# Performance work log

Hardware: AMD Instinct MI355X
Metric: run time of the kernel (lower is better)

The kernel has to match this reference:

```python
import jax, jax.numpy as jnp
import numpy as np
import math

DIM = 1024
P0 = 512          # num_stored_patterns
H = 16            # num_heads
HD = DIM // H     # head_dim = 64
STEPS = 3
B, S = 2, 1024
NEG = -1e9


def sparsemax(z):
    # sort descending along last axis
    z_sorted = -jnp.sort(-z, axis=-1)
    z_cumsum = jnp.cumsum(z_sorted, axis=-1)
    k = jnp.arange(1, z.shape[-1] + 1, dtype=z.dtype)
    support = (1 + k * z_sorted > z_cumsum).astype(z.dtype)
    k_max = support.sum(axis=-1, keepdims=True)
    idx = jnp.clip(k_max - 1, 0, None).astype(jnp.int32)
    tau = (jnp.take_along_axis(z_cumsum, idx, axis=-1) - 1.0) / jnp.maximum(k_max, 1.0)
    return jnp.clip(z - tau, 0.0, None)


def setup_inputs() -> dict:
    key = jax.random.key(0)
    ks = jax.random.split(key, 12)
    z_real = jax.random.normal(ks[0], (B, S, DIM), dtype=jnp.float32)
    z_imag = jax.random.normal(ks[1], (B, S, DIM), dtype=jnp.float32)
    # causal additive mask over dynamic (sequence) patterns
    mask = jnp.where(jnp.tril(jnp.ones((S, S), dtype=bool)), 0.0, NEG).astype(jnp.float32)
    sc = 1.0 / math.sqrt(DIM)
    stored_patterns = jax.random.normal(ks[2], (P0, DIM), dtype=jnp.float32) * 0.02
    Wq = jax.random.normal(ks[3], (DIM, DIM), dtype=jnp.float32) * sc
    Wk = jax.random.normal(ks[4], (DIM, DIM), dtype=jnp.float32) * sc
    Wv = jax.random.normal(ks[5], (DIM, DIM), dtype=jnp.float32) * sc
    Wo = jax.random.normal(ks[6], (2 * DIM, DIM), dtype=jnp.float32) * sc
    bo = jnp.zeros((2 * DIM,), dtype=jnp.float32)
    log_temp = jax.random.normal(ks[7], (H,), dtype=jnp.float32) * 0.1  # temperature=1 -> log 0
    gamma = jnp.ones((2 * DIM,), dtype=jnp.float32)
    beta = jnp.zeros((2 * DIM,), dtype=jnp.float32)
    return {"z_real": z_real, "z_imag": z_imag, "mask": mask,
            "stored_patterns": stored_patterns, "Wq": Wq, "Wk": Wk, "Wv": Wv,
            "Wo": Wo, "bo": bo, "log_temp": log_temp, "gamma": gamma, "beta": beta}


def reference(z_real, z_imag, mask, stored_patterns, Wq, Wk, Wv, Wo, bo, log_temp, gamma, beta):
    Bz, Sz, D = z_real.shape
    mag = jnp.sqrt(z_real * z_real + z_imag * z_imag)           # |z| -> dynamic patterns
    learned = jnp.broadcast_to(stored_patterns[None], (Bz, P0, D))
    patterns = jnp.concatenate([learned, mag], axis=1)          # (B, P0+S, D)
    Pt = patterns.shape[1]
    q = (mag @ Wq.T).reshape(Bz, Sz, H, HD).transpose(0, 2, 1, 3)       # (B,H,S,hd)
    k = (patterns @ Wk.T).reshape(Bz, Pt, H, HD).transpose(0, 2, 1, 3)  # (B,H,P,hd)
    v = (patterns @ Wv.T).reshape(Bz, Pt, H, HD).transpose(0, 2, 1, 3)
    temp = jnp.exp(jnp.clip(log_temp, -4.0, 4.0)).reshape(1, H, 1, 1)
    inv_scale = 1.0 / (math.sqrt(HD) * temp)
    # full additive mask: zeros over learned patterns, causal over dynamic
    full_mask = jnp.concatenate([jnp.zeros((Sz, P0), dtype=mask.dtype), mask], axis=-1)  # (S, Pt)
    state = q
    for _ in range(STEPS):
        scores = jnp.einsum('bhsd,bhpd->bhsp', state, k) * inv_scale
        scores = scores + full_mask[None, None]
        weights = sparsemax(scores)
        state = jnp.einsum('bhsp,bhpd->bhsd', weights, v)
    retrieved = state.transpose(0, 2, 1, 3).reshape(Bz, Sz, D)
    out = retrieved @ Wo.T + bo                                  # (B,S,2D)
    mu = out.mean(axis=-1, keepdims=True)
    var = out.var(axis=-1, keepdims=True)
    out = (out - mu) / jnp.sqrt(var + 1e-5) * gamma + beta
    # complex output = out[..., :D] + 1j*out[..., D:]; returned packed as (B,S,2D) real
    return out
```

## Files before the change

kernel.cpp:

```cpp
#include <hip/hip_runtime.h>
#include <math.h>

#define DIM 1024
#define P0 512
#define H 16
#define HD 64
#define B 2
#define S 1024
#define PT 1536

typedef __attribute__((ext_vector_type(8))) short short8v;
typedef __attribute__((ext_vector_type(4))) float f32x4;
typedef __attribute__((ext_vector_type(8))) unsigned short ushort8v;
typedef __attribute__((ext_vector_type(4))) unsigned short ushort4v;

__device__ __forceinline__ unsigned short bf16_rne(float x) {
  unsigned u = __builtin_bit_cast(unsigned, x);
  u += 0x7FFFu + ((u >> 16) & 1u);
  return (unsigned short)(u >> 16);
}
__device__ __forceinline__ float bf16_f(unsigned short h) {
  unsigned u = ((unsigned)h) << 16;
  return __builtin_bit_cast(float, u);
}

__global__ __launch_bounds__(256) void k_mag(const float* __restrict__ zr,
                                             const float* __restrict__ zi,
                                             float* __restrict__ mag, int n4) {
  int i = blockIdx.x * blockDim.x + threadIdx.x;
  if (i < n4) {
    float4 a = ((const float4*)zr)[i];
    float4 b = ((const float4*)zi)[i];
    float4 o;
    o.x = sqrtf(a.x * a.x + b.x * b.x);
    o.y = sqrtf(a.y * a.y + b.y * b.y);
    o.z = sqrtf(a.z * a.z + b.z * b.z);
    o.w = sqrtf(a.w * a.w + b.w * b.w);
    ((float4*)mag)[i] = o;
  }
}

__global__ __launch_bounds__(256) void k_patt(const float* __restrict__ stored,
                                              const float* __restrict__ mag,
                                              float* __restrict__ patt, int n4) {
  int i = blockIdx.x * blockDim.x + threadIdx.x;
  if (i < n4) {
    int d4 = i & (DIM / 4 - 1);
    int p  = (i >> 8) % PT;
    int b  = i / (PT * (DIM / 4));
    float4 v;
    if (p < P0) {
      v = ((const float4*)stored)[(size_t)p * (DIM / 4) + d4];
    } else {
      v = ((const float4*)mag)[((size_t)(b * S + (p - P0))) * (DIM / 4) + d4];
    }
    ((float4*)patt)[i] = v;
  }
}

__global__ __launch_bounds__(256) void k_split_plain(const float* __restrict__ X,
                                                     unsigned short* __restrict__ hi,
                                                     unsigned short* __restrict__ lo,
                                                     int n4) {
  int i = blockIdx.x * 256 + threadIdx.x;
  if (i >= n4) return;
  float4 v = ((const float4*)X)[(size_t)i];
  float xs[4] = {v.x, v.y, v.z, v.w};
  ushort4v hv, lv;
#pragma unroll
  for (int j = 0; j < 4; ++j) {
    unsigned short hb = bf16_rne(xs[j]);
    hv[j] = hb;
    lv[j] = bf16_rne(xs[j] - bf16_f(hb));
  }
  ((ushort4v*)hi)[(size_t)i] = hv;
  ((ushort4v*)lo)[(size_t)i] = lv;
}

__global__ __launch_bounds__(256, 2) void k_gemm_mfma(
    const unsigned short* __restrict__ Ah, const unsigned short* __restrict__ Al,
    const unsigned short* __restrict__ Wh, const unsigned short* __restrict__ Wl,
    const float* __restrict__ bias, float* __restrict__ Cf,
    unsigned short* __restrict__ Ohi, unsigned short* __restrict__ Olo,
    int M, int N, int K, int mode, int rpb, int aremap) {
  __shared__ short8v lds[4][4 * 132];
  const int t = threadIdx.x;
  const int w = t >> 6, lane = t & 63;
  const int l16 = lane & 15, l4 = lane >> 4;
  const int wr = w >> 1, wc = w & 1;
  const int bm = blockIdx.y, bn = blockIdx.x;

  f32x4 acc[4][4];
#pragma unroll
  for (int mi = 0; mi < 4; ++mi)
#pragma unroll
    for (int nj = 0; nj < 4; ++nj) acc[mi][nj] = (f32x4){0.f, 0.f, 0.f, 0.f};

  for (int k0 = 0; k0 < K; k0 += 32) {
    __syncthreads();
#pragma unroll
    for (int rep = 0; rep < 2; ++rep) {
      int u = rep * 256 + t;
      int kb = u & 3, r = u >> 2;
      int agr = bm * 128 + r;
      int ar = aremap ? (agr + 512 + ((agr >> 10) << 9)) : agr;
      size_t ga = (size_t)ar * K + k0 + kb * 8;
      size_t gw = (size_t)(bn * 128 + r) * K + k0 + kb * 8;
      int li = kb * 132 + r;
      lds[0][li] = *(const short8v*)(Ah + ga);
      lds[1][li] = *(const short8v*)(Al + ga);
      lds[2][li] = *(const short8v*)(Wh + gw);
      lds[3][li] = *(const short8v*)(Wl + gw);
    }
    __syncthreads();
    short8v af[4][2], bf[4][2];
#pragma unroll
    for (int mi = 0; mi < 4; ++mi) {
      int li = l4 * 132 + wr * 64 + mi * 16 + l16;
      af[mi][0] = lds[0][li];
      af[mi][1] = lds[1][li];
    }
#pragma unroll
    for (int nj = 0; nj < 4; ++nj) {
      int li = l4 * 132 + wc * 64 + nj * 16 + l16;
      bf[nj][0] = lds[2][li];
      bf[nj][1] = lds[3][li];
    }
#pragma unroll
    for (int mi = 0; mi < 4; ++mi)
#pragma unroll
      for (int nj = 0; nj < 4; ++nj) {
        acc[mi][nj] = __builtin_amdgcn_mfma_f32_16x16x32_bf16(af[mi][0], bf[nj][0], acc[mi][nj], 0, 0, 0);
        acc[mi][nj] = __builtin_amdgcn_mfma_f32_16x16x32_bf16(af[mi][0], bf[nj][1], acc[mi][nj], 0, 0, 0);
        acc[mi][nj] = __builtin_amdgcn_mfma_f32_16x16x32_bf16(af[mi][1], bf[nj][0], acc[mi][nj], 0, 0, 0);
      }
  }

#pragma unroll
  for (int mi = 0; mi < 4; ++mi)
#pragma unroll
    for (int nj = 0; nj < 4; ++nj)
#pragma unroll
      for (int i = 0; i < 4; ++i) {
        int rg = bm * 128 + wr * 64 + mi * 16 + l4 * 4 + i;
        int c  = bn * 128 + wc * 64 + nj * 16 + l16;
        float v = acc[mi][nj][i];
        if (mode == 0) {
          Cf[(size_t)rg * N + c] = v + (bias ? bias[c] : 0.f);
        } else {
          int b = rg >= rpb ? 1 : 0;
          int p = rg - b * rpb;
          int hh = c >> 6, d = c & 63;
          size_t o = (mode == 1)
                         ? ((((size_t)(b * 16 + hh)) * rpb + p) * 64 + d)
                         : ((((size_t)(b * 16 + hh)) * 64 + d) * (size_t)rpb + p);
          unsigned short hb = bf16_rne(v);
          Ohi[o] = hb;
          Olo[o] = bf16_rne(v - bf16_f(hb));
        }
      }
}

#define WSTR 40

__global__ __launch_bounds__(512, 4) void k_attn_mfma(
    const unsigned short* __restrict__ shi, const unsigned short* __restrict__ slo,
    const unsigned short* __restrict__ khi, const unsigned short* __restrict__ klo,
    const unsigned short* __restrict__ vthi, const unsigned short* __restrict__ vtlo,
    const float* __restrict__ log_temp,
    unsigned short* __restrict__ swhi, unsigned short* __restrict__ swlo,
    unsigned short* __restrict__ ohi, unsigned short* __restrict__ olo) {
  __shared__ float part[8][2][2][20];
  __shared__ unsigned short wbufh[8][16 * WSTR];
  __shared__ unsigned short wbufl[8][16 * WSTR];
  __shared__ float red2[8][16][20];
  const int t = threadIdx.x;
  const int w = t >> 6, lane = t & 63;
  const int l16 = lane & 15, l4 = lane >> 4;
  const int bid = blockIdx.x;
  const int tile = (bid & 7) * 256 + (bid >> 3);
  const int stile = tile & 63;
  const int bh = tile >> 6;
  const int h = bh & 15;
  const int s0 = stile * 16;
  const int maxTile = stile + 33;

  float lt = log_temp[h];
  lt = fminf(fmaxf(lt, -4.f), 4.f);
  const float inv_scale = 1.f / (8.f * expf(lt));

  const size_t arow = ((size_t)bh * S + s0 + l16) * HD + 8 * l4;
  short8v ahi0 = *(const short8v*)(shi + arow);
  short8v ahi1 = *(const short8v*)(shi + arow + 32);
  short8v alo0 = *(const short8v*)(slo + arow);
  short8v alo1 = *(const short8v*)(slo + arow + 32);

  const size_t kb = (size_t)bh * PT * HD;
  const size_t vb = (size_t)bh * HD * PT;
  const int sg = s0 + l16;

  float z0[6][4], z1[6][4];
#pragma unroll
  for (int j = 0; j < 6; ++j) {
    const int tA = w + 16 * j, tB = tA + 8;
    if (tA > maxTile) {
#pragma unroll
      for (int i = 0; i < 4; ++i) { z0[j][i] = -1e9f; z1[j][i] = -1e9f; }
    } else {
      const size_t k0 = kb + ((size_t)(tA * 16 + l16)) * HD + 8 * l4;
      f32x4 a0 = {0.f, 0.f, 0.f, 0.f};
      {
        short8v b00 = *(const short8v*)(khi + k0);
        short8v b01 = *(const short8v*)(khi + k0 + 32);
        short8v c00 = *(const short8v*)(klo + k0);
        short8v c01 = *(const short8v*)(klo + k0 + 32);
        a0 = __builtin_amdgcn_mfma_f32_16x16x32_bf16(b00, ahi0, a0, 0, 0, 0);
        a0 = __builtin_amdgcn_mfma_f32_16x16x32_bf16(b01, ahi1, a0, 0, 0, 0);
        a0 = __builtin_amdgcn_mfma_f32_16x16x32_bf16(b00, alo0, a0, 0, 0, 0);
        a0 = __builtin_amdgcn_mfma_f32_16x16x32_bf16(b01, alo1, a0, 0, 0, 0);
        a0 = __builtin_amdgcn_mfma_f32_16x16x32_bf16(c00, ahi0, a0, 0, 0, 0);
        a0 = __builtin_amdgcn_mfma_f32_16x16x32_bf16(c01, ahi1, a0, 0, 0, 0);
      }
#pragma unroll
      for (int i = 0; i < 4; ++i) {
        const int pA = tA * 16 + l4 * 4 + i;
        z0[j][i] = (pA > P0 + sg) ? -1e9f : a0[i] * inv_scale;
      }
      if (tB <= maxTile) {
        const size_t k1 = kb + ((size_t)(tB * 16 + l16)) * HD + 8 * l4;
        f32x4 a1 = {0.f, 0.f, 0.f, 0.f};
        short8v b10 = *(const short8v*)(khi + k1);
        short8v b11 = *(const short8v*)(khi + k1 + 32);
        short8v c10 = *(const short8v*)(klo + k1);
        short8v c11 = *(const short8v*)(klo + k1 + 32);
        a1 = __builtin_amdgcn_mfma_f32_16x16x32_bf16(b10, ahi0, a1, 0, 0, 0);
        a1 = __builtin_amdgcn_mfma_f32_16x16x32_bf16(b11, ahi1, a1, 0, 0, 0);
        a1 = __builtin_amdgcn_mfma_f32_16x16x32_bf16(b10, alo0, a1, 0, 0, 0);
        a1 = __builtin_amdgcn_mfma_f32_16x16x32_bf16(b11, alo1, a1, 0, 0, 0);
        a1 = __builtin_amdgcn_mfma_f32_16x16x32_bf16(c10, ahi0, a1, 0, 0, 0);
        a1 = __builtin_amdgcn_mfma_f32_16x16x32_bf16(c11, ahi1, a1, 0, 0, 0);
#pragma unroll
        for (int i = 0; i < 4; ++i) {
          const int pB = tB * 16 + l4 * 4 + i;
          z1[j][i] = (pB > P0 + sg) ? -1e9f : a1[i] * inv_scale;
        }
      } else {
#pragma unroll
        for (int i = 0; i < 4; ++i) z1[j][i] = -1e9f;
      }
    }
  }

  float mxv = -1e30f;
#pragma unroll
  for (int j = 0; j < 6; ++j) {
    if (w + 16 * j <= maxTile) {
#pragma unroll
      for (int i = 0; i < 4; ++i) mxv = fmaxf(mxv, fmaxf(z0[j][i], z1[j][i]));
    }
  }
  mxv = fmaxf(mxv, __shfl_xor(mxv, 16, 64));
  mxv = fmaxf(mxv, __shfl_xor(mxv, 32, 64));
  if (lane < 16) part[w][0][0][lane] = mxv;
  __syncthreads();
  float gm = -1e30f;
#pragma unroll
  for (int ww = 0; ww < 8; ++ww) gm = fmaxf(gm, part[ww][0][0][l16]);
  float tlo = gm - 1.f, thi = gm;

  for (int it = 0; it < 10; ++it) {
    const int sl = (it + 1) & 1;
    const float mid = 0.5f * (tlo + thi);
    float s = 0.f;
#pragma unroll
    for (int j = 0; j < 6; ++j) {
      if (w + 16 * j <= maxTile) {
#pragma unroll
        for (int i = 0; i < 4; ++i)
          s += fmaxf(z0[j][i] - mid, 0.f) + fmaxf(z1[j][i] - mid, 0.f);
      }
    }
    s += __shfl_xor(s, 16, 64);
    s += __shfl_xor(s, 32, 64);
    if (lane < 16) part[w][sl][0][lane] = s;
    __syncthreads();
    float rs = 0.f;
#pragma unroll
    for (int ww = 0; ww < 8; ++ww) rs += part[ww][sl][0][l16];
    if (rs >= 1.f) tlo = mid; else thi = mid;
  }

  float tau = tlo;
  for (int it = 0; it < 4; ++it) {
    const int sl = (11 + it) & 1;
    float c = 0.f, s = 0.f;
#pragma unroll
    for (int j = 0; j < 6; ++j) {
      if (w + 16 * j <= maxTile) {
#pragma unroll
        for (int i = 0; i < 4; ++i) {
          float a = z0[j][i];
          if (a > tau) { c += 1.f; s += a; }
          float b2 = z1[j][i];
          if (b2 > tau) { c += 1.f; s += b2; }
        }
      }
    }
    c += __shfl_xor(c, 16, 64);
    c += __shfl_xor(c, 32, 64);
    s += __shfl_xor(s, 16, 64);
    s += __shfl_xor(s, 32, 64);
    if (lane < 16) {
      part[w][sl][0][lane] = c;
      part[w][sl][1][lane] = s;
    }
    __syncthreads();
    float rc = 0.f, rs = 0.f;
#pragma unroll
    for (int ww = 0; ww < 8; ++ww) {
      rc += part[ww][sl][0][l16];
      rs += part[ww][sl][1][l16];
    }
    tau = (rs - 1.f) / rc;
  }

  f32x4 acc[4];
#pragma unroll
  for (int dt = 0; dt < 4; ++dt) acc[dt] = (f32x4){0.f, 0.f, 0.f, 0.f};
  unsigned short* wh = wbufh[w];
  unsigned short* wl = wbufl[w];
#pragma unroll
  for (int kk = 0; kk < 6; ++kk) {
    const int tA = w + 16 * kk, tB = tA + 8;
    if (tA > maxTile) continue;
    ushort4v h0v, l0v, h1v, l1v;
#pragma unroll
    for (int i = 0; i < 4; ++i) {
      float w0 = fmaxf(z0[kk][i] - tau, 0.f);
      float w1 = fmaxf(z1[kk][i] - tau, 0.f);
      unsigned short hb0 = bf16_rne(w0);
      unsigned short hb1 = bf16_rne(w1);
      h0v[i] = hb0; l0v[i] = bf16_rne(w0 - bf16_f(hb0));
      h1v[i] = hb1; l1v[i] = bf16_rne(w1 - bf16_f(hb1));
    }
    *(ushort4v*)(wh + l16 * WSTR + l4 * 4) = h0v;
    *(ushort4v*)(wh + l16 * WSTR + 16 + l4 * 4) = h1v;
    *(ushort4v*)(wl + l16 * WSTR + l4 * 4) = l0v;
    *(ushort4v*)(wl + l16 * WSTR + 16 + l4 * 4) = l1v;
    asm volatile("s_waitcnt lgkmcnt(0)" ::: "memory");
    __builtin_amdgcn_sched_barrier(0);
    short8v wah = *(const short8v*)(wh + l16 * WSTR + 8 * l4);
    short8v wal = *(const short8v*)(wl + l16 * WSTR + 8 * l4);
    const int pbase = (l4 < 2) ? (tA * 16 + 8 * l4) : (tB * 16 + 8 * (l4 - 2));
#pragma unroll
    for (int dt = 0; dt < 4; ++dt) {
      const size_t vo = vb + (size_t)(dt * 16 + l16) * PT + pbase;
      short8v vh = *(const short8v*)(vthi + vo);
      short8v vl = *(const short8v*)(vtlo + vo);
      acc[dt] = __builtin_amdgcn_mfma_f32_16x16x32_bf16(wah, vh, acc[dt], 0, 0, 0);
      acc[dt] = __builtin_amdgcn_mfma_f32_16x16x32_bf16(wah, vl, acc[dt], 0, 0, 0);
      acc[dt] = __builtin_amdgcn_mfma_f32_16x16x32_bf16(wal, vh, acc[dt], 0, 0, 0);
    }
  }

  for (int dt = 0; dt < 4; ++dt) {
    __syncthreads();
#pragma unroll
    for (int i = 0; i < 4; ++i)
      red2[w][l4 * 4 + i][l16] = acc[dt][i];
    __syncthreads();
    if (t < 256) {
      const int row = t >> 4, d16 = t & 15;
      float sum = 0.f;
#pragma unroll
      for (int ww = 0; ww < 8; ++ww) sum += red2[ww][row][d16];
      const int d = dt * 16 + d16;
      const int sgr = s0 + row;
      unsigned short hb = bf16_rne(sum);
      unsigned short lb = bf16_rne(sum - bf16_f(hb));
      const size_t rw = ((size_t)((bh >> 4) * S + sgr)) * DIM + h * HD + d;
      swhi[rw] = hb;
      swlo[rw] = lb;
      const size_t oi = ((size_t)bh * S + sgr) * HD + d;
      ohi[oi] = hb;
      olo[oi] = lb;
    }
  }
}

__global__ __launch_bounds__(256) void k_layernorm(float* __restrict__ out,
                                                   const float* __restrict__ gamma,
                                                   const float* __restrict__ beta) {
  const int W = 2 * DIM;
  const int r = blockIdx.x;
  float* row = out + (size_t)r * W;
  const int t = threadIdx.x;
  float4 vals[2];
  float sum = 0.f, sq = 0.f;
#pragma unroll
  for (int i = 0; i < 2; ++i) {
    float4 v = *(const float4*)(row + (i * 256 + t) * 4);
    vals[i] = v;
    sum += v.x + v.y + v.z + v.w;
    sq += v.x * v.x + v.y * v.y + v.z * v.z + v.w * v.w;
  }
#pragma unroll
  for (int off = 32; off >= 1; off >>= 1) {
    sum += __shfl_xor(sum, off, 64);
    sq  += __shfl_xor(sq,  off, 64);
  }
  __shared__ float rs[4], rq[4];
  const int wave = t >> 6, lane = t & 63;
  if (lane == 0) { rs[wave] = sum; rq[wave] = sq; }
  __syncthreads();
  sum = rs[0] + rs[1] + rs[2] + rs[3];
  sq  = rq[0] + rq[1] + rq[2] + rq[3];
  const float mean = sum / W;
  const float var = sq / W - mean * mean;
  const float rstd = rsqrtf(var + 1e-5f);
#pragma unroll
  for (int i = 0; i < 2; ++i) {
    int base = (i * 256 + t) * 4;
    float4 v = vals[i];
    float4 g = *(const float4*)(gamma + base);
    float4 bb = *(const float4*)(beta + base);
    v.x = (v.x - mean) * rstd * g.x + bb.x;
    v.y = (v.y - mean) * rstd * g.y + bb.y;
    v.z = (v.z - mean) * rstd * g.z + bb.z;
    v.w = (v.w - mean) * rstd * g.w + bb.w;
    *(float4*)(row + base) = v;
  }
}

extern "C" void kernel_launch(void* const* d_in, const int* in_sizes, int n_in,
                              void* d_out, int out_size, void* d_ws, size_t ws_size,
                              hipStream_t stream) {
  const float* zr       = (const float*)d_in[0];
  const float* zi       = (const float*)d_in[1];
  const float* stored   = (const float*)d_in[3];
  const float* Wq       = (const float*)d_in[4];
  const float* Wk       = (const float*)d_in[5];
  const float* Wv       = (const float*)d_in[6];
  const float* Wo       = (const float*)d_in[7];
  const float* bo       = (const float*)d_in[8];
  const float* log_temp = (const float*)d_in[9];
  const float* gamma    = (const float*)d_in[10];
  const float* beta     = (const float*)d_in[11];
  float* out = (float*)d_out;

  char* base = (char*)d_ws;
  float* patt = (float*)(base + (size_t)0);
  unsigned short* vthi = (unsigned short*)(base + (size_t)0);
  unsigned short* vtlo = (unsigned short*)(base + (6u << 20));
  unsigned short* phi  = (unsigned short*)(base + (12u << 20));
  unsigned short* plo  = (unsigned short*)(base + (18u << 20));
  unsigned short* swhi = (unsigned short*)(base + (12u << 20));
  unsigned short* swlo = (unsigned short*)(base + (16u << 20));
  unsigned short* wqh  = (unsigned short*)(base + (24u << 20));
  unsigned short* wql  = (unsigned short*)(base + (26u << 20));
  unsigned short* wkh  = (unsigned short*)(base + (28u << 20));
  unsigned short* wkl  = (unsigned short*)(base + (30u << 20));
  unsigned short* wvh  = (unsigned short*)(base + (32u << 20));
  unsigned short* wvl  = (unsigned short*)(base + (34u << 20));
  unsigned short* woh  = (unsigned short*)(base + (24u << 20));
  unsigned short* wol  = (unsigned short*)(base + (28u << 20));
  float* mag = (float*)(base + (36u << 20));
  unsigned short* qhi = (unsigned short*)(base + (36u << 20));
  unsigned short* qlo = (unsigned short*)(base + (40u << 20));
  unsigned short* s1hi = (unsigned short*)(base + (44u << 20));
  unsigned short* s1lo = (unsigned short*)(base + (48u << 20));
  unsigned short* khi  = (unsigned short*)(base + (52u << 20));
  unsigned short* klo  = (unsigned short*)(base + (58u << 20));

  const int n4 = B * S * DIM / 4;
  k_mag<<<(n4 + 255) / 256, 256, 0, stream>>>(zr, zi, mag, n4);
  const int p4 = B * PT * DIM / 4;
  k_patt<<<(p4 + 255) / 256, 256, 0, stream>>>(stored, mag, patt, p4);

  k_split_plain<<<p4 / 256, 256, 0, stream>>>(patt, phi, plo, p4);
  const int w4 = DIM * DIM / 4;
  k_split_plain<<<w4 / 256, 256, 0, stream>>>(Wq, wqh, wql, w4);
  k_split_plain<<<w4 / 256, 256, 0, stream>>>(Wk, wkh, wkl, w4);
  k_split_plain<<<w4 / 256, 256, 0, stream>>>(Wv, wvh, wvl, w4);

  dim3 gq(1024 / 128, 2048 / 128);
  k_gemm_mfma<<<gq, 256, 0, stream>>>(phi, plo, wqh, wql, nullptr, nullptr,
                                      qhi, qlo, 2048, 1024, 1024, 1, 1024, 1);
  dim3 gkv(1024 / 128, 3072 / 128);
  k_gemm_mfma<<<gkv, 256, 0, stream>>>(phi, plo, wkh, wkl, nullptr, nullptr,
                                       khi, klo, 3072, 1024, 1024, 1, 1536, 0);
  k_gemm_mfma<<<gkv, 256, 0, stream>>>(phi, plo, wvh, wvl, nullptr, nullptr,
                                       vthi, vtlo, 3072, 1024, 1024, 2, 1536, 0);

  const int wo4 = 2 * DIM * DIM / 4;
  k_split_plain<<<wo4 / 256, 256, 0, stream>>>(Wo, woh, wol, wo4);

  const int ablocks = B * H * (S / 16);
  k_attn_mfma<<<ablocks, 512, 0, stream>>>(qhi, qlo, khi, klo, vthi, vtlo,
                                           log_temp, swhi, swlo, s1hi, s1lo);
  k_attn_mfma<<<ablocks, 512, 0, stream>>>(s1hi, s1lo, khi, klo, vthi, vtlo,
                                           log_temp, swhi, swlo, qhi, qlo);
  k_attn_mfma<<<ablocks, 512, 0, stream>>>(qhi, qlo, khi, klo, vthi, vtlo,
                                           log_temp, swhi, swlo, s1hi, s1lo);

  dim3 go(2048 / 128, 2048 / 128);
  k_gemm_mfma<<<go, 256, 0, stream>>>(swhi, swlo, woh, wol, bo, out,
                                      nullptr, nullptr, 2048, 2048, 1024, 0, 0, 0);
  k_layernorm<<<B * S, 256, 0, stream>>>(out, gamma, beta);
}
```

Measured before the change: 748.0 us.

## Fuse pattern concat with bf16 split and use 4-way threshold search in sparsemax

Merges the pattern-concatenation kernel with the hi/lo bf16 split so the fp32 pattern buffer is never written and reread. Replaces the 10-iteration bisection for the sparsemax threshold with 4 rounds that each test 4 candidate thresholds (5-way split), which cuts block-wide barriers and reduction rounds but adds more arithmetic per round. Also raises the attention kernel's launch-bounds waves hint from 4 to 6, which may force register spills. The coarser search narrows the bracket less (0.2^4 vs 2^-10) before the refinement loop, which relies on the following exact-support iterations to converge.

After: 979.8 us. 1.31x slower.

```diff
diff --git a/kernel.cpp b/kernel.cpp
--- a/kernel.cpp
+++ b/kernel.cpp
@@ -40,22 +40,32 @@
   }
 }
 
-__global__ __launch_bounds__(256) void k_patt(const float* __restrict__ stored,
-                                              const float* __restrict__ mag,
-                                              float* __restrict__ patt, int n4) {
+__global__ __launch_bounds__(256) void k_patt_split(const float* __restrict__ stored,
+                                                    const float* __restrict__ mag,
+                                                    unsigned short* __restrict__ phi,
+                                                    unsigned short* __restrict__ plo,
+                                                    int n4) {
   int i = blockIdx.x * blockDim.x + threadIdx.x;
-  if (i < n4) {
-    int d4 = i & (DIM / 4 - 1);
-    int p  = (i >> 8) % PT;
-    int b  = i / (PT * (DIM / 4));
-    float4 v;
-    if (p < P0) {
-      v = ((const float4*)stored)[(size_t)p * (DIM / 4) + d4];
-    } else {
-      v = ((const float4*)mag)[((size_t)(b * S + (p - P0))) * (DIM / 4) + d4];
-    }
-    ((float4*)patt)[i] = v;
-  }
+  if (i >= n4) return;
+  int d4 = i & (DIM / 4 - 1);
+  int p  = (i >> 8) % PT;
+  int b  = i / (PT * (DIM / 4));
+  float4 v;
+  if (p < P0) {
+    v = ((const float4*)stored)[(size_t)p * (DIM / 4) + d4];
+  } else {
+    v = ((const float4*)mag)[((size_t)(b * S + (p - P0))) * (DIM / 4) + d4];
+  }
+  float xs[4] = {v.x, v.y, v.z, v.w};
+  ushort4v hv, lv;
+#pragma unroll
+  for (int j = 0; j < 4; ++j) {
+    unsigned short hb = bf16_rne(xs[j]);
+    hv[j] = hb;
+    lv[j] = bf16_rne(xs[j] - bf16_f(hb));
+  }
+  ((ushort4v*)phi)[(size_t)i] = hv;
+  ((ushort4v*)plo)[(size_t)i] = lv;
 }
 
 __global__ __launch_bounds__(256) void k_split_plain(const float* __restrict__ X,
@@ -163,14 +173,14 @@
 
 #define WSTR 40
 
-__global__ __launch_bounds__(512, 4) void k_attn_mfma(
+__global__ __launch_bounds__(512, 6) void k_attn_mfma(
     const unsigned short* __restrict__ shi, const unsigned short* __restrict__ slo,
     const unsigned short* __restrict__ khi, const unsigned short* __restrict__ klo,
     const unsigned short* __restrict__ vthi, const unsigned short* __restrict__ vtlo,
     const float* __restrict__ log_temp,
     unsigned short* __restrict__ swhi, unsigned short* __restrict__ swlo,
     unsigned short* __restrict__ ohi, unsigned short* __restrict__ olo) {
-  __shared__ float part[8][2][2][20];
+  __shared__ float part[8][2][4][20];
   __shared__ unsigned short wbufh[8][16 * WSTR];
   __shared__ unsigned short wbufl[8][16 * WSTR];
   __shared__ float red2[8][16][20];
@@ -266,33 +276,51 @@
   float gm = -1e30f;
 #pragma unroll
   for (int ww = 0; ww < 8; ++ww) gm = fmaxf(gm, part[ww][0][0][l16]);
-  float tlo = gm - 1.f, thi = gm;
-
-  for (int it = 0; it < 10; ++it) {
+  float tlo = gm - 1.f;
+  float wdt = 1.f;
+
+  for (int it = 0; it < 4; ++it) {
     const int sl = (it + 1) & 1;
-    const float mid = 0.5f * (tlo + thi);
-    float s = 0.f;
+    const float step = wdt * 0.2f;
+    float cand[4], sums[4];
+#pragma unroll
+    for (int k = 0; k < 4; ++k) { cand[k] = tlo + step * (k + 1); sums[k] = 0.f; }
 #pragma unroll
     for (int j = 0; j < 6; ++j) {
       if (w + 16 * j <= maxTile) {
 #pragma unroll
-        for (int i = 0; i < 4; ++i)
-          s += fmaxf(z0[j][i] - mid, 0.f) + fmaxf(z1[j][i] - mid, 0.f);
-      }
-    }
-    s += __shfl_xor(s, 16, 64);
-    s += __shfl_xor(s, 32, 64);
-    if (lane < 16) part[w][sl][0][lane] = s;
+        for (int i = 0; i < 4; ++i) {
+          const float a = z0[j][i], b2 = z1[j][i];
+#pragma unroll
+          for (int k = 0; k < 4; ++k)
+            sums[k] += fmaxf(a - cand[k], 0.f) + fmaxf(b2 - cand[k], 0.f);
+        }
+      }
+    }
+#pragma unroll
+    for (int k = 0; k < 4; ++k) {
+      sums[k] += __shfl_xor(sums[k], 16, 64);
+      sums[k] += __shfl_xor(sums[k], 32, 64);
+    }
+    if (lane < 16) {
+#pragma unroll
+      for (int k = 0; k < 4; ++k) part[w][sl][k][lane] = sums[k];
+    }
     __syncthreads();
-    float rs = 0.f;
-#pragma unroll
-    for (int ww = 0; ww < 8; ++ww) rs += part[ww][sl][0][l16];
-    if (rs >= 1.f) tlo = mid; else thi = mid;
+    float rs[4] = {0.f, 0.f, 0.f, 0.f};
+#pragma unroll
+    for (int ww = 0; ww < 8; ++ww)
+#pragma unroll
+      for (int k = 0; k < 4; ++k) rs[k] += part[ww][sl][k][l16];
+#pragma unroll
+    for (int k = 0; k < 4; ++k)
+      if (rs[k] >= 1.f) tlo = cand[k];
+    wdt = step;
   }
 
   float tau = tlo;
   for (int it = 0; it < 4; ++it) {
-    const int sl = (11 + it) & 1;
+    const int sl = (5 + it) & 1;
     float c = 0.f, s = 0.f;
 #pragma unroll
     for (int j = 0; j < 6; ++j) {
@@ -449,7 +477,6 @@
   float* out = (float*)d_out;
 
   char* base = (char*)d_ws;
-  float* patt = (float*)(base + (size_t)0);
   unsigned short* vthi = (unsigned short*)(base + (size_t)0);
   unsigned short* vtlo = (unsigned short*)(base + (6u << 20));
   unsigned short* phi  = (unsigned short*)(base + (12u << 20));
@@ -475,9 +502,8 @@
   const int n4 = B * S * DIM / 4;
   k_mag<<<(n4 + 255) / 256, 256, 0, stream>>>(zr, zi, mag, n4);
   const int p4 = B * PT * DIM / 4;
-  k_patt<<<(p4 + 255) / 256, 256, 0, stream>>>(stored, mag, patt, p4);
-
-  k_split_plain<<<p4 / 256, 256, 0, stream>>>(patt, phi, plo, p4);
+  k_patt_split<<<(p4 + 255) / 256, 256, 0, stream>>>(stored, mag, phi, plo, p4);
+
   const int w4 = DIM * DIM / 4;
   k_split_plain<<<w4 / 256, 256, 0, stream>>>(Wq, wqh, wql, w4);
   k_split_plain<<<w4 / 256, 256, 0, stream>>>(Wk, wkh, wkl, w4);
```

## Fuse pattern concat with bf16 split, shuffle weights, cut bisection iterations

Applied to the files above, without the earlier changes.

Merges the pattern-concatenation kernel with the hi/lo bf16 split, so the fp32 pattern buffer is never written and read back. In the attention kernel, the sparsemax weights are rearranged into MFMA operand layout with cross-lane shuffles instead of a round trip through LDS, which frees the wbuf shared arrays. The tau bisection drops from 10 to 6 iterations before the Newton-style refinement, and the reductions use split accumulators for more instruction-level parallelism. Fewer bisection steps leave a coarser starting tau, which could change accuracy if the 4 refinement steps do not converge.

New measurement: 709.9 us. 5.1% less time.

```diff
diff --git a/kernel.cpp b/kernel.cpp
--- a/kernel.cpp
+++ b/kernel.cpp
@@ -13,6 +13,8 @@
 typedef __attribute__((ext_vector_type(4))) float f32x4;
 typedef __attribute__((ext_vector_type(8))) unsigned short ushort8v;
 typedef __attribute__((ext_vector_type(4))) unsigned short ushort4v;
+typedef unsigned long long ull;
+struct ull2 { ull a, b; };
 
 __device__ __forceinline__ unsigned short bf16_rne(float x) {
   unsigned u = __builtin_bit_cast(unsigned, x);
@@ -40,22 +42,32 @@
   }
 }
 
-__global__ __launch_bounds__(256) void k_patt(const float* __restrict__ stored,
-                                              const float* __restrict__ mag,
-                                              float* __restrict__ patt, int n4) {
+__global__ __launch_bounds__(256) void k_patt_split(const float* __restrict__ stored,
+                                                    const float* __restrict__ mag,
+                                                    unsigned short* __restrict__ phi,
+                                                    unsigned short* __restrict__ plo,
+                                                    int n4) {
   int i = blockIdx.x * blockDim.x + threadIdx.x;
-  if (i < n4) {
-    int d4 = i & (DIM / 4 - 1);
-    int p  = (i >> 8) % PT;
-    int b  = i / (PT * (DIM / 4));
-    float4 v;
-    if (p < P0) {
-      v = ((const float4*)stored)[(size_t)p * (DIM / 4) + d4];
-    } else {
-      v = ((const float4*)mag)[((size_t)(b * S + (p - P0))) * (DIM / 4) + d4];
-    }
-    ((float4*)patt)[i] = v;
-  }
+  if (i >= n4) return;
+  int d4 = i & (DIM / 4 - 1);
+  int p  = (i >> 8) % PT;
+  int b  = i / (PT * (DIM / 4));
+  float4 v;
+  if (p < P0) {
+    v = ((const float4*)stored)[(size_t)p * (DIM / 4) + d4];
+  } else {
+    v = ((const float4*)mag)[((size_t)(b * S + (p - P0))) * (DIM / 4) + d4];
+  }
+  float xs[4] = {v.x, v.y, v.z, v.w};
+  ushort4v hv, lv;
+#pragma unroll
+  for (int j = 0; j < 4; ++j) {
+    unsigned short hb = bf16_rne(xs[j]);
+    hv[j] = hb;
+    lv[j] = bf16_rne(xs[j] - bf16_f(hb));
+  }
+  ((ushort4v*)phi)[(size_t)i] = hv;
+  ((ushort4v*)plo)[(size_t)i] = lv;
 }
 
 __global__ __launch_bounds__(256) void k_split_plain(const float* __restrict__ X,
@@ -161,8 +173,6 @@
       }
 }
 
-#define WSTR 40
-
 __global__ __launch_bounds__(512, 4) void k_attn_mfma(
     const unsigned short* __restrict__ shi, const unsigned short* __restrict__ slo,
     const unsigned short* __restrict__ khi, const unsigned short* __restrict__ klo,
@@ -171,8 +181,6 @@
     unsigned short* __restrict__ swhi, unsigned short* __restrict__ swlo,
     unsigned short* __restrict__ ohi, unsigned short* __restrict__ olo) {
   __shared__ float part[8][2][2][20];
-  __shared__ unsigned short wbufh[8][16 * WSTR];
-  __shared__ unsigned short wbufl[8][16 * WSTR];
   __shared__ float red2[8][16][20];
   const int t = threadIdx.x;
   const int w = t >> 6, lane = t & 63;
@@ -251,14 +259,18 @@
     }
   }
 
-  float mxv = -1e30f;
+  float mA = -1e30f, mB = -1e30f;
 #pragma unroll
   for (int j = 0; j < 6; ++j) {
     if (w + 16 * j <= maxTile) {
 #pragma unroll
-      for (int i = 0; i < 4; ++i) mxv = fmaxf(mxv, fmaxf(z0[j][i], z1[j][i]));
-    }
-  }
+      for (int i = 0; i < 4; ++i) {
+        mA = fmaxf(mA, z0[j][i]);
+        mB = fmaxf(mB, z1[j][i]);
+      }
+    }
+  }
+  float mxv = fmaxf(mA, mB);
   mxv = fmaxf(mxv, __shfl_xor(mxv, 16, 64));
   mxv = fmaxf(mxv, __shfl_xor(mxv, 32, 64));
   if (lane < 16) part[w][0][0][lane] = mxv;
@@ -268,18 +280,21 @@
   for (int ww = 0; ww < 8; ++ww) gm = fmaxf(gm, part[ww][0][0][l16]);
   float tlo = gm - 1.f, thi = gm;
 
-  for (int it = 0; it < 10; ++it) {
+  for (int it = 0; it < 6; ++it) {
     const int sl = (it + 1) & 1;
     const float mid = 0.5f * (tlo + thi);
-    float s = 0.f;
+    float sa = 0.f, sb = 0.f;
 #pragma unroll
     for (int j = 0; j < 6; ++j) {
       if (w + 16 * j <= maxTile) {
 #pragma unroll
-        for (int i = 0; i < 4; ++i)
-          s += fmaxf(z0[j][i] - mid, 0.f) + fmaxf(z1[j][i] - mid, 0.f);
-      }
-    }
+        for (int i = 0; i < 4; ++i) {
+          sa += fmaxf(z0[j][i] - mid, 0.f);
+          sb += fmaxf(z1[j][i] - mid, 0.f);
+        }
+      }
+    }
+    float s = sa + sb;
     s += __shfl_xor(s, 16, 64);
     s += __shfl_xor(s, 32, 64);
     if (lane < 16) part[w][sl][0][lane] = s;
@@ -292,20 +307,21 @@
 
   float tau = tlo;
   for (int it = 0; it < 4; ++it) {
-    const int sl = (11 + it) & 1;
-    float c = 0.f, s = 0.f;
+    const int sl = (7 + it) & 1;
+    float ca = 0.f, cb = 0.f, sa = 0.f, sb = 0.f;
 #pragma unroll
     for (int j = 0; j < 6; ++j) {
       if (w + 16 * j <= maxTile) {
 #pragma unroll
         for (int i = 0; i < 4; ++i) {
           float a = z0[j][i];
-          if (a > tau) { c += 1.f; s += a; }
+          if (a > tau) { ca += 1.f; sa += a; }
           float b2 = z1[j][i];
-          if (b2 > tau) { c += 1.f; s += b2; }
+          if (b2 > tau) { cb += 1.f; sb += b2; }
         }
       }
     }
+    float c = ca + cb, s = sa + sb;
     c += __shfl_xor(c, 16, 64);
     c += __shfl_xor(c, 32, 64);
     s += __shfl_xor(s, 16, 64);
@@ -327,8 +343,6 @@
   f32x4 acc[4];
 #pragma unroll
   for (int dt = 0; dt < 4; ++dt) acc[dt] = (f32x4){0.f, 0.f, 0.f, 0.f};
-  unsigned short* wh = wbufh[w];
-  unsigned short* wl = wbufl[w];
 #pragma unroll
   for (int kk = 0; kk < 6; ++kk) {
     const int tA = w + 16 * kk, tB = tA + 8;
@@ -343,14 +357,24 @@
       h0v[i] = hb0; l0v[i] = bf16_rne(w0 - bf16_f(hb0));
       h1v[i] = hb1; l1v[i] = bf16_rne(w1 - bf16_f(hb1));
     }
-    *(ushort4v*)(wh + l16 * WSTR + l4 * 4) = h0v;
-    *(ushort4v*)(wh + l16 * WSTR + 16 + l4 * 4) = h1v;
-    *(ushort4v*)(wl + l16 * WSTR + l4 * 4) = l0v;
-    *(ushort4v*)(wl + l16 * WSTR + 16 + l4 * 4) = l1v;
-    asm volatile("s_waitcnt lgkmcnt(0)" ::: "memory");
-    __builtin_amdgcn_sched_barrier(0);
-    short8v wah = *(const short8v*)(wh + l16 * WSTR + 8 * l4);
-    short8v wal = *(const short8v*)(wl + l16 * WSTR + 8 * l4);
+    const ull P0v = __builtin_bit_cast(ull, h0v);
+    const ull P1v = __builtin_bit_cast(ull, h1v);
+    const ull Q0v = __builtin_bit_cast(ull, l0v);
+    const ull Q1v = __builtin_bit_cast(ull, l1v);
+    const int srcA = l16 + 16 * (2 * (l4 & 1));
+    const int srcB = srcA + 16;
+    ull a0 = __shfl(P0v, srcA, 64);
+    ull a1 = __shfl(P1v, srcA, 64);
+    ull b0 = __shfl(P0v, srcB, 64);
+    ull b1 = __shfl(P1v, srcB, 64);
+    ull qa0 = __shfl(Q0v, srcA, 64);
+    ull qa1 = __shfl(Q1v, srcA, 64);
+    ull qb0 = __shfl(Q0v, srcB, 64);
+    ull qb1 = __shfl(Q1v, srcB, 64);
+    ull2 th = { (l4 < 2) ? a0 : a1, (l4 < 2) ? b0 : b1 };
+    ull2 tl = { (l4 < 2) ? qa0 : qa1, (l4 < 2) ? qb0 : qb1 };
+    short8v wah = __builtin_bit_cast(short8v, th);
+    short8v wal = __builtin_bit_cast(short8v, tl);
     const int pbase = (l4 < 2) ? (tA * 16 + 8 * l4) : (tB * 16 + 8 * (l4 - 2));
 #pragma unroll
     for (int dt = 0; dt < 4; ++dt) {
@@ -449,7 +473,6 @@
   float* out = (float*)d_out;
 
   char* base = (char*)d_ws;
-  float* patt = (float*)(base + (size_t)0);
   unsigned short* vthi = (unsigned short*)(base + (size_t)0);
   unsigned short* vtlo = (unsigned short*)(base + (6u << 20));
   unsigned short* phi  = (unsigned short*)(base + (12u << 20));
@@ -475,9 +498,8 @@
   const int n4 = B * S * DIM / 4;
   k_mag<<<(n4 + 255) / 256, 256, 0, stream>>>(zr, zi, mag, n4);
   const int p4 = B * PT * DIM / 4;
-  k_patt<<<(p4 + 255) / 256, 256, 0, stream>>>(stored, mag, patt, p4);
-
-  k_split_plain<<<p4 / 256, 256, 0, stream>>>(patt, phi, plo, p4);
+  k_patt_split<<<(p4 + 255) / 256, 256, 0, stream>>>(stored, mag, phi, plo, p4);
+
   const int w4 = DIM * DIM / 4;
   k_split_plain<<<w4 / 256, 256, 0, stream>>>(Wq, wqh, wql, w4);
   k_split_plain<<<w4 / 256, 256, 0, stream>>>(Wk, wkh, wkl, w4);
```
